# Kernel optimization log

Measured on AMD Instinct MI355X. Metric: run time of the kernel, lower is better.

## Reference

```python
import jax, jax.numpy as jnp
import numpy as np

N, E, IN, H, D = 100000, 1600000, 128, 4, 64
NEG_SLOPE = 0.2
K_APPNP, ALPHA = 5, 0.5
BN_EPS = 1e-5


def setup_inputs() -> dict:
    key = jax.random.key(0)
    ks = jax.random.split(key, 12)
    return {
        'node_feats': jax.random.normal(ks[0], (N, IN), jnp.float32),
        'src': jax.random.randint(ks[1], (E,), 0, N, jnp.int32),
        'dst': jax.random.randint(ks[2], (E,), 0, N, jnp.int32),
        'W_fc': jax.random.normal(ks[3], (IN, H * D), jnp.float32) * (1.0 / np.sqrt(IN)),
        'attn_l': jax.random.normal(ks[4], (H, D), jnp.float32) * 0.1,
        'attn_r': jax.random.normal(ks[5], (H, D), jnp.float32) * 0.1,
        'W_res_gat': jax.random.normal(ks[6], (IN, H * D), jnp.float32) * (1.0 / np.sqrt(IN)),
        'gat_bias': jax.random.normal(ks[7], (H * D,), jnp.float32) * 0.01,
        'conv_w': jax.random.normal(ks[8], (1, H), jnp.float32) * 0.5,
        'conv_b': jax.random.normal(ks[9], (1,), jnp.float32) * 0.01,
        'W_res': jax.random.normal(ks[10], (D, IN), jnp.float32) * (1.0 / np.sqrt(IN)),
        'b_res': jax.random.normal(ks[11], (D,), jnp.float32) * 0.01,
        'gamma': jnp.ones((D,), jnp.float32),
        'beta': jnp.zeros((D,), jnp.float32),
    }


def reference(node_feats, src, dst, W_fc, attn_l, attn_r, W_res_gat, gat_bias,
              conv_w, conv_b, W_res, b_res, gamma, beta):
    # ---- GATConv (4 heads, residual, relu) ----
    feat = (node_feats @ W_fc).reshape(N, H, D)            # (N,H,D)
    el = jnp.einsum('nhd,hd->nh', feat, attn_l)            # (N,H)
    er = jnp.einsum('nhd,hd->nh', feat, attn_r)
    e = jax.nn.leaky_relu(el[src] + er[dst], NEG_SLOPE)    # (E,H)
    # edge softmax over incoming edges of each dst node
    emax = jax.ops.segment_max(e, dst, num_segments=N)     # (N,H)
    emax = jnp.where(jnp.isfinite(emax), emax, 0.0)
    ee = jnp.exp(e - emax[dst])                            # (E,H)
    denom = jax.ops.segment_sum(ee, dst, num_segments=N)   # (N,H)
    a = ee / jnp.maximum(denom[dst], 1e-9)                 # (E,H)
    msg = feat[src] * a[..., None]                         # (E,H,D)
    rst = jax.ops.segment_sum(msg, dst, num_segments=N)    # (N,H,D)
    resval = (node_feats @ W_res_gat).reshape(N, H, D)
    rst = jax.nn.relu(rst + resval + gat_bias.reshape(1, H, D))
    # ---- Conv1d (heads -> 1, kernel_size=1) then flatten ----
    h = jnp.einsum('nhd,oh->nod', rst, conv_w) + conv_b[None, :, None]
    h = h.reshape(N, D)
    # ---- APPNP (k=5, alpha=0.5), symmetric deg^{-1/2} norm (in-degree, clamp 1) ----
    deg = jax.ops.segment_sum(jnp.ones((E,), jnp.float32), dst, num_segments=N)
    norm = jnp.power(jnp.maximum(deg, 1.0), -0.5)[:, None]  # (N,1)
    h0 = h
    for _ in range(K_APPNP):
        h = jax.ops.segment_sum((h * norm)[src], dst, num_segments=N) * norm
        h = (1.0 - ALPHA) * h + ALPHA * h0
    # ---- residual linear + relu ----
    h = h + jax.nn.relu(node_feats @ W_res.T + b_res)
    # ---- BatchNorm1d (batch stats, affine) ----
    mu = h.mean(axis=0)
    var = h.var(axis=0)
    return (h - mu) * jax.lax.rsqrt(var + BN_EPS) * gamma + beta
```

## Files before the change

kernel.cpp:

```cpp
#include <hip/hip_runtime.h>
#include <math.h>

#define NN 100000
#define NE 1600000
#define NEG_SLOPE 0.2f

typedef __attribute__((ext_vector_type(8))) short bf16x8;
typedef __attribute__((ext_vector_type(4))) float f32x4;
typedef __attribute__((ext_vector_type(2))) float f32x2;

__device__ __forceinline__ float b2f(unsigned short u) {
  union { unsigned u; float f; } c; c.u = ((unsigned)u) << 16; return c.f;
}
__device__ __forceinline__ unsigned short f2b(float x) {
  union { float f; unsigned u; } c; c.f = x;
  unsigned r = c.u + 0x7FFFu + ((c.u >> 16) & 1u);
  return (unsigned short)(r >> 16);
}
__device__ __forceinline__ float readlane_f(float v, int l) {
  return __uint_as_float((unsigned)__builtin_amdgcn_readlane((int)__float_as_uint(v), l));
}
__device__ __forceinline__ void fma4(float4& acc, float s, const float4& b) {
  acc.x = fmaf(s, b.x, acc.x);
  acc.y = fmaf(s, b.y, acc.y);
  acc.z = fmaf(s, b.z, acc.z);
  acc.w = fmaf(s, b.w, acc.w);
}
__device__ __forceinline__ float wred(float v) {
#pragma unroll
  for (int off = 32; off > 0; off >>= 1) v += __shfl_xor(v, off, 64);
  return v;
}

__global__ __launch_bounds__(256) void k_zero(int* __restrict__ p, int nwords) {
  int i = blockIdx.x * 256 + threadIdx.x;
  if (i < nwords) p[i] = 0;
}

__global__ void k_zrow(unsigned short* __restrict__ a, unsigned short* __restrict__ b) {
  int i = threadIdx.x;
  a[(size_t)NN * 64 + i] = 0;
  b[(size_t)NN * 64 + i] = 0;
}

__global__ __launch_bounds__(256) void k_cast(const float* __restrict__ A, unsigned short* __restrict__ Ab) {
  int i = blockIdx.x * 256 + threadIdx.x;
  int i4 = i * 4;
  if (i4 < NN * 128) {
    float4 v = *(const float4*)&A[i4];
    ushort4 o; o.x = f2b(v.x); o.y = f2b(v.y); o.z = f2b(v.z); o.w = f2b(v.w);
    *(ushort4*)&Ab[i4] = o;
  }
}

__global__ __launch_bounds__(256) void k_deg(const int* __restrict__ dst, int* __restrict__ deg) {
  int i = blockIdx.x * 256 + threadIdx.x;
  if (i < NE) atomicAdd(&deg[dst[i]], 1);
}

__global__ __launch_bounds__(256) void k_alloc(const int* __restrict__ deg, int* __restrict__ row_start,
                                               int* __restrict__ counter, float* __restrict__ nrm) {
  int i = blockIdx.x * 256 + threadIdx.x;
  if (i < NN) {
    row_start[i] = atomicAdd(counter, deg[i]);
    nrm[i] = rsqrtf(fmaxf((float)deg[i], 1.0f));
  }
}

__global__ __launch_bounds__(256) void k_scatter(const int* __restrict__ src, const int* __restrict__ dst,
                                                 const int* __restrict__ row_start, int* __restrict__ cursor,
                                                 int* __restrict__ csr_src) {
  int i = blockIdx.x * 256 + threadIdx.x;
  if (i < NE) {
    int n = dst[i];
    int p = atomicAdd(&cursor[n], 1);
    csr_src[row_start[n] + p] = src[i];
  }
}

__global__ __launch_bounds__(256) void k_prepw(const float* __restrict__ W_fc, const float* __restrict__ al,
                                               const float* __restrict__ ar, float* __restrict__ w) {
  int o = blockIdx.x * 256 + threadIdx.x;
  if (o >= 1024) return;
  int side = o >> 9;
  int h = (o >> 7) & 3;
  int k = o & 127;
  const float* a = side ? ar : al;
  float s = 0.f;
  for (int d = 0; d < 64; ++d) s += W_fc[k * 256 + h * 64 + d] * a[h * 64 + d];
  w[(side * 4 + h) * 128 + k] = s;
}

__global__ __launch_bounds__(256) void k_elr2(const float* __restrict__ X, const float* __restrict__ w,
                                              float* __restrict__ el, float* __restrict__ er) {
  int n = blockIdx.x * 32 + (threadIdx.x >> 3);
  int p = threadIdx.x & 7;
  if (n >= NN) return;
  const float4* xr = (const float4*)(X + (size_t)n * 128);
  const float4* wr = (const float4*)(w + p * 128);
  float s = 0.f;
#pragma unroll
  for (int i = 0; i < 32; ++i) {
    float4 x = xr[i], ww = wr[i];
    s += x.x * ww.x + x.y * ww.y + x.z * ww.z + x.w * ww.w;
  }
  if (p < 4) el[n * 4 + p] = s;
  else er[n * 4 + (p - 4)] = s;
}

__global__ __launch_bounds__(256) void k_prepB(const float* __restrict__ W_fc, const float* __restrict__ W_rg,
                                               unsigned short* __restrict__ Bp) {
  int y = blockIdx.y;
  const float* Bsrc = (y >> 1) ? W_rg : W_fc;
  int colbase = (y & 1) * 128;
  for (int e = blockIdx.x * 256 + threadIdx.x; e < 16384; e += 2048) {
    int n = e & 127, k = e >> 7;
    int p = colbase + n;
    int d = p >> 2, hh = p & 3;
    float v = Bsrc[k * 256 + hh * 64 + d];
    int nt = n >> 4, nn = n & 15, kt = k >> 5, quad = (k >> 3) & 3, j = k & 7;
    Bp[(size_t)y * 16384 + ((nt * 4 + kt) * 64 + quad * 16 + nn) * 8 + j] = f2b(v);
  }
}

__global__ __launch_bounds__(256) void k_gemm_mfma(const unsigned short* __restrict__ Abf,
                                                   const unsigned short* __restrict__ Bp,
                                                   unsigned* __restrict__ feat8u,
                                                   unsigned short* __restrict__ resval2) {
  __shared__ unsigned short Bl[16384];
  int tid = threadIdx.x;
  int half = blockIdx.y >> 1;
  int colbase = (blockIdx.y & 1) * 128;
  {
    const uint4* src = (const uint4*)(Bp + (size_t)blockIdx.y * 16384);
    uint4* dst4 = (uint4*)Bl;
#pragma unroll
    for (int i = 0; i < 8; ++i) dst4[tid + i * 256] = src[tid + i * 256];
  }
  __syncthreads();
  int w = tid >> 6, lane = tid & 63;
  int quad = lane >> 4;
  int row0 = blockIdx.x * 128;
  int mrow = row0 + (lane & 15);
  f32x4 acc[8][2];
#pragma unroll
  for (int rt = 0; rt < 8; ++rt)
#pragma unroll
    for (int c = 0; c < 2; ++c) acc[rt][c] = (f32x4){0.f, 0.f, 0.f, 0.f};
#pragma unroll
  for (int kt = 0; kt < 4; ++kt) {
    bf16x8 b0 = *(const bf16x8*)&Bl[(((w * 2 + 0) * 4 + kt) * 64 + lane) * 8];
    bf16x8 b1 = *(const bf16x8*)&Bl[(((w * 2 + 1) * 4 + kt) * 64 + lane) * 8];
    int kb = kt * 32 + quad * 8;
#pragma unroll
    for (int rt = 0; rt < 8; ++rt) {
      int rr = mrow + rt * 16; if (rr > NN - 1) rr = NN - 1;
      bf16x8 a = *(const bf16x8*)&Abf[(size_t)rr * 128 + kb];
      acc[rt][0] = __builtin_amdgcn_mfma_f32_16x16x32_bf16(b0, a, acc[rt][0], 0, 0, 0);
      acc[rt][1] = __builtin_amdgcn_mfma_f32_16x16x32_bf16(b1, a, acc[rt][1], 0, 0, 0);
    }
  }
#pragma unroll
  for (int rt = 0; rt < 8; ++rt) {
    int m = row0 + rt * 16 + (lane & 15);
    if (m < NN) {
#pragma unroll
      for (int c = 0; c < 2; ++c) {
        int col = colbase + (w * 2 + c) * 16 + quad * 4;
        if (half == 0) {
          int pk = __builtin_amdgcn_cvt_pk_fp8_f32(acc[rt][c][0], acc[rt][c][1], 0, false);
          pk = __builtin_amdgcn_cvt_pk_fp8_f32(acc[rt][c][2], acc[rt][c][3], pk, true);
          feat8u[(size_t)m * 64 + (col >> 2)] = (unsigned)pk;
        } else {
          ushort4 o;
          o.x = f2b(acc[rt][c][0]); o.y = f2b(acc[rt][c][1]);
          o.z = f2b(acc[rt][c][2]); o.w = f2b(acc[rt][c][3]);
          *(ushort4*)&resval2[(size_t)m * 256 + col] = o;
        }
      }
    }
  }
}

__global__ __launch_bounds__(256) void k_gemm_nt_bias_relu(const float* __restrict__ A, const float* __restrict__ B,
                                                           const float* __restrict__ bias, float* __restrict__ C) {
  __shared__ float Bl[128][68];
  for (int idx = threadIdx.x; idx < 64 * 128; idx += 256) {
    int d = idx >> 7, k = idx & 127;
    Bl[k][d] = B[d * 128 + k];
  }
  __syncthreads();
  int tx = threadIdx.x & 15, ty = threadIdx.x >> 4;
  int row0 = blockIdx.x * 64 + ty * 4;
  const float* ap[4];
#pragma unroll
  for (int r = 0; r < 4; ++r) ap[r] = A + (size_t)min(row0 + r, NN - 1) * 128;
  float4 acc[4];
#pragma unroll
  for (int r = 0; r < 4; ++r) acc[r] = make_float4(0.f, 0.f, 0.f, 0.f);
#pragma unroll 2
  for (int k0 = 0; k0 < 128; k0 += 4) {
    float4 b0 = *(const float4*)&Bl[k0][tx * 4];
    float4 b1 = *(const float4*)&Bl[k0 + 1][tx * 4];
    float4 b2 = *(const float4*)&Bl[k0 + 2][tx * 4];
    float4 b3 = *(const float4*)&Bl[k0 + 3][tx * 4];
#pragma unroll
    for (int r = 0; r < 4; ++r) {
      float4 a = *(const float4*)(ap[r] + k0);
      fma4(acc[r], a.x, b0); fma4(acc[r], a.y, b1);
      fma4(acc[r], a.z, b2); fma4(acc[r], a.w, b3);
    }
  }
  float4 bv = *(const float4*)&bias[tx * 4];
#pragma unroll
  for (int r = 0; r < 4; ++r) {
    int row = row0 + r;
    if (row < NN) {
      float4 v;
      v.x = fmaxf(acc[r].x + bv.x, 0.f);
      v.y = fmaxf(acc[r].y + bv.y, 0.f);
      v.z = fmaxf(acc[r].z + bv.z, 0.f);
      v.w = fmaxf(acc[r].w + bv.w, 0.f);
      *(float4*)&C[(size_t)row * 64 + tx * 4] = v;
    }
  }
}

__global__ __launch_bounds__(256) void k_gat(const int* __restrict__ row_start, const int* __restrict__ deg,
                                             const int* __restrict__ csr_src, const float* __restrict__ el,
                                             const float* __restrict__ er, const unsigned* __restrict__ feat8u,
                                             const unsigned short* __restrict__ resval2,
                                             const float* __restrict__ gat_bias, const float* __restrict__ conv_w,
                                             const float* __restrict__ conv_b, const float* __restrict__ nrm,
                                             float* __restrict__ h0, unsigned short* __restrict__ hsA) {
  int n = blockIdx.x * 4 + (threadIdx.x >> 6);
  int lane = threadIdx.x & 63;
  if (n >= NN) return;
  int s0 = row_start[n], cnt = deg[n];
  float4 er4 = *(const float4*)&er[n * 4];
  f32x2 acc01 = (f32x2){0.f, 0.f}, acc23 = (f32x2){0.f, 0.f};
  float den0 = 0.f, den1 = 0.f, den2 = 0.f, den3 = 0.f;
  for (int base = 0; base < cnt; base += 64) {
    int j = base + lane;
    int s = 0;
    float x0 = 0.f, x1 = 0.f, x2 = 0.f, x3 = 0.f;
    if (j < cnt) {
      s = csr_src[s0 + j];
      float4 el4 = *(const float4*)&el[s * 4];
      float e0 = el4.x + er4.x; e0 = (e0 > 0.f) ? e0 : NEG_SLOPE * e0;
      float e1 = el4.y + er4.y; e1 = (e1 > 0.f) ? e1 : NEG_SLOPE * e1;
      float e2 = el4.z + er4.z; e2 = (e2 > 0.f) ? e2 : NEG_SLOPE * e2;
      float e3 = el4.w + er4.w; e3 = (e3 > 0.f) ? e3 : NEG_SLOPE * e3;
      x0 = __expf(e0); x1 = __expf(e1); x2 = __expf(e2); x3 = __expf(e3);
      den0 += x0; den1 += x1; den2 += x2; den3 += x3;
    }
    int m = cnt - base; if (m > 64) m = 64;
    int mr = (m + 3) & ~3;
    for (int t = 0; t < mr; t += 4) {
      int ss0 = __builtin_amdgcn_readlane(s, t);
      int ss1 = __builtin_amdgcn_readlane(s, t + 1);
      int ss2 = __builtin_amdgcn_readlane(s, t + 2);
      int ss3 = __builtin_amdgcn_readlane(s, t + 3);
      unsigned f0 = feat8u[(size_t)ss0 * 64 + lane];
      unsigned f1 = feat8u[(size_t)ss1 * 64 + lane];
      unsigned f2 = feat8u[(size_t)ss2 * 64 + lane];
      unsigned f3 = feat8u[(size_t)ss3 * 64 + lane];
      {
        f32x2 a01 = (f32x2){readlane_f(x0, t), readlane_f(x1, t)};
        f32x2 a23 = (f32x2){readlane_f(x2, t), readlane_f(x3, t)};
        f32x2 lo = __builtin_amdgcn_cvt_pk_f32_fp8((int)f0, false);
        f32x2 hi = __builtin_amdgcn_cvt_pk_f32_fp8((int)f0, true);
        acc01 += a01 * lo; acc23 += a23 * hi;
      }
      {
        f32x2 a01 = (f32x2){readlane_f(x0, t + 1), readlane_f(x1, t + 1)};
        f32x2 a23 = (f32x2){readlane_f(x2, t + 1), readlane_f(x3, t + 1)};
        f32x2 lo = __builtin_amdgcn_cvt_pk_f32_fp8((int)f1, false);
        f32x2 hi = __builtin_amdgcn_cvt_pk_f32_fp8((int)f1, true);
        acc01 += a01 * lo; acc23 += a23 * hi;
      }
      {
        f32x2 a01 = (f32x2){readlane_f(x0, t + 2), readlane_f(x1, t + 2)};
        f32x2 a23 = (f32x2){readlane_f(x2, t + 2), readlane_f(x3, t + 2)};
        f32x2 lo = __builtin_amdgcn_cvt_pk_f32_fp8((int)f2, false);
        f32x2 hi = __builtin_amdgcn_cvt_pk_f32_fp8((int)f2, true);
        acc01 += a01 * lo; acc23 += a23 * hi;
      }
      {
        f32x2 a01 = (f32x2){readlane_f(x0, t + 3), readlane_f(x1, t + 3)};
        f32x2 a23 = (f32x2){readlane_f(x2, t + 3), readlane_f(x3, t + 3)};
        f32x2 lo = __builtin_amdgcn_cvt_pk_f32_fp8((int)f3, false);
        f32x2 hi = __builtin_amdgcn_cvt_pk_f32_fp8((int)f3, true);
        acc01 += a01 * lo; acc23 += a23 * hi;
      }
    }
  }
  den0 = wred(den0); den1 = wred(den1); den2 = wred(den2); den3 = wred(den3);
  float i0 = 1.f / fmaxf(den0, 1e-9f);
  float i1 = 1.f / fmaxf(den1, 1e-9f);
  float i2 = 1.f / fmaxf(den2, 1e-9f);
  float i3 = 1.f / fmaxf(den3, 1e-9f);
  ushort4 rv = *(const ushort4*)&resval2[(size_t)n * 256 + lane * 4];
  float hmix = conv_b[0];
  float t0;
  t0 = fmaf(acc01.x, i0, b2f(rv.x) + gat_bias[lane]);       t0 = fmaxf(t0, 0.f); hmix = fmaf(conv_w[0], t0, hmix);
  t0 = fmaf(acc01.y, i1, b2f(rv.y) + gat_bias[64 + lane]);  t0 = fmaxf(t0, 0.f); hmix = fmaf(conv_w[1], t0, hmix);
  t0 = fmaf(acc23.x, i2, b2f(rv.z) + gat_bias[128 + lane]); t0 = fmaxf(t0, 0.f); hmix = fmaf(conv_w[2], t0, hmix);
  t0 = fmaf(acc23.y, i3, b2f(rv.w) + gat_bias[192 + lane]); t0 = fmaxf(t0, 0.f); hmix = fmaf(conv_w[3], t0, hmix);
  size_t o = (size_t)n * 64 + lane;
  h0[o] = hmix;
  hsA[o] = f2b(hmix * nrm[n]);
}

__global__ __launch_bounds__(256) void k_gather_mid(const int* __restrict__ row_start, const int* __restrict__ deg,
                                                    const int* __restrict__ csr_src,
                                                    const unsigned short* __restrict__ hs_in,
                                                    const float* __restrict__ nrm, const float* __restrict__ h0,
                                                    unsigned short* __restrict__ hs_out) {
  int n = blockIdx.x * 4 + (threadIdx.x >> 6);
  int lane = threadIdx.x & 63;
  if (n >= NN) return;
  int s0 = row_start[n], cnt = deg[n];
  float acc = 0.f;
  for (int base = 0; base < cnt; base += 64) {
    int j = base + lane;
    int s = (j < cnt) ? csr_src[s0 + j] : NN;
    int m = cnt - base; if (m > 64) m = 64;
    int mr = (m + 7) & ~7;
    for (int t = 0; t < mr; t += 8) {
      int ss0 = __builtin_amdgcn_readlane(s, t);
      int ss1 = __builtin_amdgcn_readlane(s, t + 1);
      int ss2 = __builtin_amdgcn_readlane(s, t + 2);
      int ss3 = __builtin_amdgcn_readlane(s, t + 3);
      int ss4 = __builtin_amdgcn_readlane(s, t + 4);
      int ss5 = __builtin_amdgcn_readlane(s, t + 5);
      int ss6 = __builtin_amdgcn_readlane(s, t + 6);
      int ss7 = __builtin_amdgcn_readlane(s, t + 7);
      float u0 = b2f(hs_in[(size_t)ss0 * 64 + lane]);
      float u1 = b2f(hs_in[(size_t)ss1 * 64 + lane]);
      float u2 = b2f(hs_in[(size_t)ss2 * 64 + lane]);
      float u3 = b2f(hs_in[(size_t)ss3 * 64 + lane]);
      float u4 = b2f(hs_in[(size_t)ss4 * 64 + lane]);
      float u5 = b2f(hs_in[(size_t)ss5 * 64 + lane]);
      float u6 = b2f(hs_in[(size_t)ss6 * 64 + lane]);
      float u7 = b2f(hs_in[(size_t)ss7 * 64 + lane]);
      acc += ((u0 + u1) + (u2 + u3)) + ((u4 + u5) + (u6 + u7));
    }
  }
  size_t o = (size_t)n * 64 + lane;
  float nn_ = nrm[n];
  float v = fmaf(0.5f * nn_, acc, 0.5f * h0[o]);
  hs_out[o] = f2b(v * nn_);
}

__global__ __launch_bounds__(256) void k_gather_last(const int* __restrict__ row_start, const int* __restrict__ deg,
                                                     const int* __restrict__ csr_src,
                                                     const unsigned short* __restrict__ hs_in,
                                                     const float* __restrict__ nrm, const float* __restrict__ h0,
                                                     unsigned short* __restrict__ hout) {
  int n = blockIdx.x * 4 + (threadIdx.x >> 6);
  int lane = threadIdx.x & 63;
  if (n >= NN) return;
  int s0 = row_start[n], cnt = deg[n];
  float acc = 0.f;
  for (int base = 0; base < cnt; base += 64) {
    int j = base + lane;
    int s = (j < cnt) ? csr_src[s0 + j] : NN;
    int m = cnt - base; if (m > 64) m = 64;
    int mr = (m + 7) & ~7;
    for (int t = 0; t < mr; t += 8) {
      int ss0 = __builtin_amdgcn_readlane(s, t);
      int ss1 = __builtin_amdgcn_readlane(s, t + 1);
      int ss2 = __builtin_amdgcn_readlane(s, t + 2);
      int ss3 = __builtin_amdgcn_readlane(s, t + 3);
      int ss4 = __builtin_amdgcn_readlane(s, t + 4);
      int ss5 = __builtin_amdgcn_readlane(s, t + 5);
      int ss6 = __builtin_amdgcn_readlane(s, t + 6);
      int ss7 = __builtin_amdgcn_readlane(s, t + 7);
      float u0 = b2f(hs_in[(size_t)ss0 * 64 + lane]);
      float u1 = b2f(hs_in[(size_t)ss1 * 64 + lane]);
      float u2 = b2f(hs_in[(size_t)ss2 * 64 + lane]);
      float u3 = b2f(hs_in[(size_t)ss3 * 64 + lane]);
      float u4 = b2f(hs_in[(size_t)ss4 * 64 + lane]);
      float u5 = b2f(hs_in[(size_t)ss5 * 64 + lane]);
      float u6 = b2f(hs_in[(size_t)ss6 * 64 + lane]);
      float u7 = b2f(hs_in[(size_t)ss7 * 64 + lane]);
      acc += ((u0 + u1) + (u2 + u3)) + ((u4 + u5) + (u6 + u7));
    }
  }
  size_t o = (size_t)n * 64 + lane;
  float v = fmaf(0.5f * nrm[n], acc, 0.5f * h0[o]);
  hout[o] = f2b(v);
}

__global__ __launch_bounds__(256) void k_finred(const unsigned short* __restrict__ hl,
                                                const float* __restrict__ res2, float* __restrict__ hfin,
                                                float* __restrict__ bn) {
  __shared__ float s1[256], s2[256];
  int d = threadIdx.x & 63;
  int rb = blockIdx.x * 64;
  float sum = 0.f, sq = 0.f;
  for (int r = threadIdx.x >> 6; r < 64; r += 4) {
    int n = rb + r;
    if (n < NN) {
      size_t idx = (size_t)n * 64 + d;
      float v = b2f(hl[idx]) + res2[idx];
      hfin[idx] = v;
      sum += v; sq += v * v;
    }
  }
  s1[threadIdx.x] = sum; s2[threadIdx.x] = sq;
  __syncthreads();
  if (threadIdx.x < 128) { s1[threadIdx.x] += s1[threadIdx.x + 128]; s2[threadIdx.x] += s2[threadIdx.x + 128]; }
  __syncthreads();
  if (threadIdx.x < 64) {
    atomicAdd(&bn[d], s1[threadIdx.x] + s1[threadIdx.x + 64]);
    atomicAdd(&bn[64 + d], s2[threadIdx.x] + s2[threadIdx.x + 64]);
  }
}

__global__ void k_bnstats(const float* __restrict__ bn, const float* __restrict__ gamma,
                          const float* __restrict__ beta, float* __restrict__ bns) {
  int d = threadIdx.x;
  float mu = bn[d] * (1.0f / NN);
  float var = fmaxf(bn[64 + d] * (1.0f / NN) - mu * mu, 0.f);
  float sc = rsqrtf(var + 1e-5f) * gamma[d];
  bns[d] = sc;
  bns[64 + d] = beta[d] - mu * sc;
}

__global__ __launch_bounds__(256) void k_bnapply(const float* __restrict__ h, const float* __restrict__ bns,
                                                 float* __restrict__ out) {
  int i = blockIdx.x * 256 + threadIdx.x;
  if (i < NN * 64) {
    int d = i & 63;
    out[i] = fmaf(h[i], bns[d], bns[64 + d]);
  }
}

extern "C" void kernel_launch(void* const* d_in, const int* in_sizes, int n_in,
                              void* d_out, int out_size, void* d_ws, size_t ws_size,
                              hipStream_t stream) {
  const float* node_feats = (const float*)d_in[0];
  const int* src = (const int*)d_in[1];
  const int* dst = (const int*)d_in[2];
  const float* W_fc = (const float*)d_in[3];
  const float* attn_l = (const float*)d_in[4];
  const float* attn_r = (const float*)d_in[5];
  const float* W_res_gat = (const float*)d_in[6];
  const float* gat_bias = (const float*)d_in[7];
  const float* conv_w = (const float*)d_in[8];
  const float* conv_b = (const float*)d_in[9];
  const float* W_res = (const float*)d_in[10];
  const float* b_res = (const float*)d_in[11];
  const float* gamma = (const float*)d_in[12];
  const float* beta = (const float*)d_in[13];
  float* out = (float*)d_out;

  char* base = (char*)d_ws;
  size_t off = 0;
  auto alloc = [&](size_t bytes) -> char* {
    char* p = base + off;
    off = (off + bytes + 255) & ~(size_t)255;
    return p;
  };
  unsigned* feat8u        = (unsigned*)alloc((size_t)NN * 256);
  unsigned short* resval2 = (unsigned short*)alloc((size_t)NN * 256 * 2);
  float* res2             = (float*)resval2;
  float* el               = (float*)alloc((size_t)NN * 4 * 4);
  float* er               = (float*)alloc((size_t)NN * 4 * 4);
  float* h0               = (float*)alloc((size_t)NN * 64 * 4);
  unsigned short* Abf     = (unsigned short*)h0;
  unsigned short* hsA     = (unsigned short*)alloc((size_t)(NN + 1) * 64 * 2);
  unsigned short* hsB     = (unsigned short*)alloc((size_t)(NN + 1) * 64 * 2);
  unsigned short* hout    = (unsigned short*)alloc((size_t)NN * 64 * 2);
  int* csr_src            = (int*)alloc((size_t)NE * 4);
  float* nrm              = (float*)alloc((size_t)NN * 4);
  int* row_start          = (int*)alloc((size_t)NN * 4);
  unsigned short* Bpacked = (unsigned short*)alloc((size_t)4 * 16384 * 2);
  float* w_elr            = (float*)alloc((size_t)8 * 128 * 4);
  size_t zoff = off;
  int* deg                = (int*)alloc((size_t)NN * 4);
  int* cursor             = (int*)alloc((size_t)NN * 4);
  int* counter            = (int*)alloc(256);
  float* bn               = (float*)alloc(256 * 4);
  float* hfin             = h0;

  int zwords = (int)((off - zoff) / 4);
  int gE = (NE + 255) / 256;
  int gN = (NN + 255) / 256;
  int gW = (NN + 3) / 4;
  int gM = (NN + 63) / 64;
  int gV = (NN * 64 + 255) / 256;

  k_zero<<<(zwords + 255) / 256, 256, 0, stream>>>((int*)(base + zoff), zwords);
  k_zrow<<<1, 64, 0, stream>>>(hsA, hsB);
  k_deg<<<gE, 256, 0, stream>>>(dst, deg);
  k_alloc<<<gN, 256, 0, stream>>>(deg, row_start, counter, nrm);
  k_scatter<<<gE, 256, 0, stream>>>(src, dst, row_start, cursor, csr_src);

  k_cast<<<(NN * 128 / 4 + 255) / 256, 256, 0, stream>>>(node_feats, Abf);
  k_prepB<<<dim3(8, 4), 256, 0, stream>>>(W_fc, W_res_gat, Bpacked);
  k_prepw<<<4, 256, 0, stream>>>(W_fc, attn_l, attn_r, w_elr);
  k_gemm_mfma<<<dim3((NN + 127) / 128, 4), 256, 0, stream>>>(Abf, Bpacked, feat8u, resval2);

  k_elr2<<<(NN + 31) / 32, 256, 0, stream>>>(node_feats, w_elr, el, er);
  k_gat<<<gW, 256, 0, stream>>>(row_start, deg, csr_src, el, er, feat8u, resval2,
                                gat_bias, conv_w, conv_b, nrm, h0, hsA);

  k_gemm_nt_bias_relu<<<gM, 256, 0, stream>>>(node_feats, W_res, b_res, res2);

  k_gather_mid<<<gW, 256, 0, stream>>>(row_start, deg, csr_src, hsA, nrm, h0, hsB);
  k_gather_mid<<<gW, 256, 0, stream>>>(row_start, deg, csr_src, hsB, nrm, h0, hsA);
  k_gather_mid<<<gW, 256, 0, stream>>>(row_start, deg, csr_src, hsA, nrm, h0, hsB);
  k_gather_mid<<<gW, 256, 0, stream>>>(row_start, deg, csr_src, hsB, nrm, h0, hsA);
  k_gather_last<<<gW, 256, 0, stream>>>(row_start, deg, csr_src, hsA, nrm, h0, hout);

  k_finred<<<gM, 256, 0, stream>>>(hout, res2, hfin, bn);
  k_bnstats<<<1, 64, 0, stream>>>(bn, gamma, beta, bn + 128);
  k_bnapply<<<gV, 256, 0, stream>>>(hfin, bn + 128, out);
}
```

Measured before the change: 841.5 us.

## Gather multiple edges per wave with wide loads and fuse residual into last hop

The GAT and APPNP gather kernels now split each wave into sub-groups that each handle a different edge. Lanes load 8-byte chunks of a neighbour row instead of one element per lane, and the per-edge source indices and attention weights are staged through LDS instead of readlane broadcasts. Partial sums are combined with cross-lane shuffles at the end. The final APPNP hop now adds the residual directly and writes fp32 in place into h0, which removes the separate bf16 hout buffer and one read/write pass from the BN reduction kernel. The LDS staging is done without explicit barriers, which relies on wave-synchronous execution within each wave's private slice.

```diff
diff --git a/kernel.cpp b/kernel.cpp
--- a/kernel.cpp
+++ b/kernel.cpp
@@ -16,9 +16,6 @@
   union { float f; unsigned u; } c; c.f = x;
   unsigned r = c.u + 0x7FFFu + ((c.u >> 16) & 1u);
   return (unsigned short)(r >> 16);
-}
-__device__ __forceinline__ float readlane_f(float v, int l) {
-  return __uint_as_float((unsigned)__builtin_amdgcn_readlane((int)__float_as_uint(v), l));
 }
 __device__ __forceinline__ void fma4(float4& acc, float s, const float4& b) {
   acc.x = fmaf(s, b.x, acc.x);
@@ -233,12 +230,17 @@
                                              const float* __restrict__ gat_bias, const float* __restrict__ conv_w,
                                              const float* __restrict__ conv_b, const float* __restrict__ nrm,
                                              float* __restrict__ h0, unsigned short* __restrict__ hsA) {
-  int n = blockIdx.x * 4 + (threadIdx.x >> 6);
-  int lane = threadIdx.x & 63;
+  __shared__ int s_src[4][64];
+  __shared__ float s_x[4][64][4];
+  int wid = threadIdx.x >> 6, lane = threadIdx.x & 63;
+  int n = blockIdx.x * 4 + wid;
   if (n >= NN) return;
   int s0 = row_start[n], cnt = deg[n];
   float4 er4 = *(const float4*)&er[n * 4];
-  f32x2 acc01 = (f32x2){0.f, 0.f}, acc23 = (f32x2){0.f, 0.f};
+  int k = lane & 31, g = lane >> 5;
+  unsigned koff = (unsigned)(k << 3);
+  f32x2 a01_0 = (f32x2){0.f, 0.f}, a23_0 = (f32x2){0.f, 0.f};
+  f32x2 a01_1 = (f32x2){0.f, 0.f}, a23_1 = (f32x2){0.f, 0.f};
   float den0 = 0.f, den1 = 0.f, den2 = 0.f, den3 = 0.f;
   for (int base = 0; base < cnt; base += 64) {
     int j = base + lane;
@@ -254,45 +256,32 @@
       x0 = __expf(e0); x1 = __expf(e1); x2 = __expf(e2); x3 = __expf(e3);
       den0 += x0; den1 += x1; den2 += x2; den3 += x3;
     }
+    s_src[wid][lane] = s;
+    *(float4*)&s_x[wid][lane][0] = make_float4(x0, x1, x2, x3);
     int m = cnt - base; if (m > 64) m = 64;
     int mr = (m + 3) & ~3;
     for (int t = 0; t < mr; t += 4) {
-      int ss0 = __builtin_amdgcn_readlane(s, t);
-      int ss1 = __builtin_amdgcn_readlane(s, t + 1);
-      int ss2 = __builtin_amdgcn_readlane(s, t + 2);
-      int ss3 = __builtin_amdgcn_readlane(s, t + 3);
-      unsigned f0 = feat8u[(size_t)ss0 * 64 + lane];
-      unsigned f1 = feat8u[(size_t)ss1 * 64 + lane];
-      unsigned f2 = feat8u[(size_t)ss2 * 64 + lane];
-      unsigned f3 = feat8u[(size_t)ss3 * 64 + lane];
-      {
-        f32x2 a01 = (f32x2){readlane_f(x0, t), readlane_f(x1, t)};
-        f32x2 a23 = (f32x2){readlane_f(x2, t), readlane_f(x3, t)};
-        f32x2 lo = __builtin_amdgcn_cvt_pk_f32_fp8((int)f0, false);
-        f32x2 hi = __builtin_amdgcn_cvt_pk_f32_fp8((int)f0, true);
-        acc01 += a01 * lo; acc23 += a23 * hi;
-      }
-      {
-        f32x2 a01 = (f32x2){readlane_f(x0, t + 1), readlane_f(x1, t + 1)};
-        f32x2 a23 = (f32x2){readlane_f(x2, t + 1), readlane_f(x3, t + 1)};
-        f32x2 lo = __builtin_amdgcn_cvt_pk_f32_fp8((int)f1, false);
-        f32x2 hi = __builtin_amdgcn_cvt_pk_f32_fp8((int)f1, true);
-        acc01 += a01 * lo; acc23 += a23 * hi;
-      }
-      {
-        f32x2 a01 = (f32x2){readlane_f(x0, t + 2), readlane_f(x1, t + 2)};
-        f32x2 a23 = (f32x2){readlane_f(x2, t + 2), readlane_f(x3, t + 2)};
-        f32x2 lo = __builtin_amdgcn_cvt_pk_f32_fp8((int)f2, false);
-        f32x2 hi = __builtin_amdgcn_cvt_pk_f32_fp8((int)f2, true);
-        acc01 += a01 * lo; acc23 += a23 * hi;
-      }
-      {
-        f32x2 a01 = (f32x2){readlane_f(x0, t + 3), readlane_f(x1, t + 3)};
-        f32x2 a23 = (f32x2){readlane_f(x2, t + 3), readlane_f(x3, t + 3)};
-        f32x2 lo = __builtin_amdgcn_cvt_pk_f32_fp8((int)f3, false);
-        f32x2 hi = __builtin_amdgcn_cvt_pk_f32_fp8((int)f3, true);
-        acc01 += a01 * lo; acc23 += a23 * hi;
-      }
+      int sA = s_src[wid][t + g];
+      int sB = s_src[wid][t + 2 + g];
+      float4 xA = *(const float4*)&s_x[wid][t + g][0];
+      float4 xB = *(const float4*)&s_x[wid][t + 2 + g][0];
+      uint2 fA = *(const uint2*)((const char*)feat8u + (((unsigned)sA << 8) + koff));
+      uint2 fB = *(const uint2*)((const char*)feat8u + (((unsigned)sB << 8) + koff));
+      f32x2 xa01 = (f32x2){xA.x, xA.y}, xa23 = (f32x2){xA.z, xA.w};
+      f32x2 xb01 = (f32x2){xB.x, xB.y}, xb23 = (f32x2){xB.z, xB.w};
+      f32x2 lo, hi;
+      lo = __builtin_amdgcn_cvt_pk_f32_fp8((int)fA.x, false);
+      hi = __builtin_amdgcn_cvt_pk_f32_fp8((int)fA.x, true);
+      a01_0 += xa01 * lo; a23_0 += xa23 * hi;
+      lo = __builtin_amdgcn_cvt_pk_f32_fp8((int)fA.y, false);
+      hi = __builtin_amdgcn_cvt_pk_f32_fp8((int)fA.y, true);
+      a01_1 += xa01 * lo; a23_1 += xa23 * hi;
+      lo = __builtin_amdgcn_cvt_pk_f32_fp8((int)fB.x, false);
+      hi = __builtin_amdgcn_cvt_pk_f32_fp8((int)fB.x, true);
+      a01_0 += xb01 * lo; a23_0 += xb23 * hi;
+      lo = __builtin_amdgcn_cvt_pk_f32_fp8((int)fB.y, false);
+      hi = __builtin_amdgcn_cvt_pk_f32_fp8((int)fB.y, true);
+      a01_1 += xb01 * lo; a23_1 += xb23 * hi;
     }
   }
   den0 = wred(den0); den1 = wred(den1); den2 = wred(den2); den3 = wred(den3);
@@ -300,16 +289,74 @@
   float i1 = 1.f / fmaxf(den1, 1e-9f);
   float i2 = 1.f / fmaxf(den2, 1e-9f);
   float i3 = 1.f / fmaxf(den3, 1e-9f);
-  ushort4 rv = *(const ushort4*)&resval2[(size_t)n * 256 + lane * 4];
-  float hmix = conv_b[0];
-  float t0;
-  t0 = fmaf(acc01.x, i0, b2f(rv.x) + gat_bias[lane]);       t0 = fmaxf(t0, 0.f); hmix = fmaf(conv_w[0], t0, hmix);
-  t0 = fmaf(acc01.y, i1, b2f(rv.y) + gat_bias[64 + lane]);  t0 = fmaxf(t0, 0.f); hmix = fmaf(conv_w[1], t0, hmix);
-  t0 = fmaf(acc23.x, i2, b2f(rv.z) + gat_bias[128 + lane]); t0 = fmaxf(t0, 0.f); hmix = fmaf(conv_w[2], t0, hmix);
-  t0 = fmaf(acc23.y, i3, b2f(rv.w) + gat_bias[192 + lane]); t0 = fmaxf(t0, 0.f); hmix = fmaf(conv_w[3], t0, hmix);
-  size_t o = (size_t)n * 64 + lane;
-  h0[o] = hmix;
-  hsA[o] = f2b(hmix * nrm[n]);
+  a01_0[0] += __shfl_xor(a01_0[0], 32, 64);
+  a01_0[1] += __shfl_xor(a01_0[1], 32, 64);
+  a23_0[0] += __shfl_xor(a23_0[0], 32, 64);
+  a23_0[1] += __shfl_xor(a23_0[1], 32, 64);
+  a01_1[0] += __shfl_xor(a01_1[0], 32, 64);
+  a01_1[1] += __shfl_xor(a01_1[1], 32, 64);
+  a23_1[0] += __shfl_xor(a23_1[0], 32, 64);
+  a23_1[1] += __shfl_xor(a23_1[1], 32, 64);
+  if (lane < 32) {
+    int d0 = k << 1;
+    uint4 rv = *(const uint4*)&resval2[(size_t)n * 256 + ((unsigned)k << 3)];
+    float2 bb0 = *(const float2*)&gat_bias[d0];
+    float2 bb1 = *(const float2*)&gat_bias[64 + d0];
+    float2 bb2 = *(const float2*)&gat_bias[128 + d0];
+    float2 bb3 = *(const float2*)&gat_bias[192 + d0];
+    float cb = conv_b[0];
+    float cw0 = conv_w[0], cw1 = conv_w[1], cw2 = conv_w[2], cw3 = conv_w[3];
+    float t, hm0 = cb, hm1 = cb;
+    t = fmaf(a01_0[0], i0, b2f((unsigned short)(rv.x & 0xffffu)) + bb0.x); t = fmaxf(t, 0.f); hm0 = fmaf(cw0, t, hm0);
+    t = fmaf(a01_0[1], i1, b2f((unsigned short)(rv.x >> 16)) + bb1.x);     t = fmaxf(t, 0.f); hm0 = fmaf(cw1, t, hm0);
+    t = fmaf(a23_0[0], i2, b2f((unsigned short)(rv.y & 0xffffu)) + bb2.x); t = fmaxf(t, 0.f); hm0 = fmaf(cw2, t, hm0);
+    t = fmaf(a23_0[1], i3, b2f((unsigned short)(rv.y >> 16)) + bb3.x);     t = fmaxf(t, 0.f); hm0 = fmaf(cw3, t, hm0);
+    t = fmaf(a01_1[0], i0, b2f((unsigned short)(rv.z & 0xffffu)) + bb0.y); t = fmaxf(t, 0.f); hm1 = fmaf(cw0, t, hm1);
+    t = fmaf(a01_1[1], i1, b2f((unsigned short)(rv.z >> 16)) + bb1.y);     t = fmaxf(t, 0.f); hm1 = fmaf(cw1, t, hm1);
+    t = fmaf(a23_1[0], i2, b2f((unsigned short)(rv.w & 0xffffu)) + bb2.y); t = fmaxf(t, 0.f); hm1 = fmaf(cw2, t, hm1);
+    t = fmaf(a23_1[1], i3, b2f((unsigned short)(rv.w >> 16)) + bb3.y);     t = fmaxf(t, 0.f); hm1 = fmaf(cw3, t, hm1);
+    float nn_ = nrm[n];
+    size_t o = (size_t)n * 64 + d0;
+    *(float2*)&h0[o] = make_float2(hm0, hm1);
+    ushort2 hs; hs.x = f2b(hm0 * nn_); hs.y = f2b(hm1 * nn_);
+    *(ushort2*)&hsA[o] = hs;
+  }
+}
+
+__device__ __forceinline__ void gather_accum(const int* __restrict__ row_start, const int* __restrict__ deg,
+                                             const int* __restrict__ csr_src,
+                                             const unsigned short* __restrict__ hs_in,
+                                             int n, int wid, int lane,
+                                             float& a0, float& a1, float& a2, float& a3) {
+  __shared__ int s_src[4][64];
+  int s0 = row_start[n], cnt = deg[n];
+  int k = lane & 15, g = lane >> 4;
+  unsigned koff = (unsigned)(k << 3);
+  a0 = 0.f; a1 = 0.f; a2 = 0.f; a3 = 0.f;
+  for (int base = 0; base < cnt; base += 64) {
+    int j = base + lane;
+    s_src[wid][lane] = (j < cnt) ? csr_src[s0 + j] : NN;
+    int m = cnt - base; if (m > 64) m = 64;
+    int mr = (m + 7) & ~7;
+    for (int t = 0; t < mr; t += 8) {
+      int sA = s_src[wid][t + g];
+      int sB = s_src[wid][t + 4 + g];
+      uint2 uA = *(const uint2*)((const char*)hs_in + (((unsigned)sA << 7) + koff));
+      uint2 uB = *(const uint2*)((const char*)hs_in + (((unsigned)sB << 7) + koff));
+      a0 += __uint_as_float(uA.x << 16);
+      a1 += __uint_as_float(uA.x & 0xFFFF0000u);
+      a2 += __uint_as_float(uA.y << 16);
+      a3 += __uint_as_float(uA.y & 0xFFFF0000u);
+      a0 += __uint_as_float(uB.x << 16);
+      a1 += __uint_as_float(uB.x & 0xFFFF0000u);
+      a2 += __uint_as_float(uB.y << 16);
+      a3 += __uint_as_float(uB.y & 0xFFFF0000u);
+    }
+  }
+  a0 += __shfl_xor(a0, 16, 64); a1 += __shfl_xor(a1, 16, 64);
+  a2 += __shfl_xor(a2, 16, 64); a3 += __shfl_xor(a3, 16, 64);
+  a0 += __shfl_xor(a0, 32, 64); a1 += __shfl_xor(a1, 32, 64);
+  a2 += __shfl_xor(a2, 32, 64); a3 += __shfl_xor(a3, 32, 64);
 }
 
 __global__ __launch_bounds__(256) void k_gather_mid(const int* __restrict__ row_start, const int* __restrict__ deg,
@@ -317,85 +364,52 @@
                                                     const unsigned short* __restrict__ hs_in,
                                                     const float* __restrict__ nrm, const float* __restrict__ h0,
                                                     unsigned short* __restrict__ hs_out) {
-  int n = blockIdx.x * 4 + (threadIdx.x >> 6);
-  int lane = threadIdx.x & 63;
+  int wid = threadIdx.x >> 6, lane = threadIdx.x & 63;
+  int n = blockIdx.x * 4 + wid;
   if (n >= NN) return;
-  int s0 = row_start[n], cnt = deg[n];
-  float acc = 0.f;
-  for (int base = 0; base < cnt; base += 64) {
-    int j = base + lane;
-    int s = (j < cnt) ? csr_src[s0 + j] : NN;
-    int m = cnt - base; if (m > 64) m = 64;
-    int mr = (m + 7) & ~7;
-    for (int t = 0; t < mr; t += 8) {
-      int ss0 = __builtin_amdgcn_readlane(s, t);
-      int ss1 = __builtin_amdgcn_readlane(s, t + 1);
-      int ss2 = __builtin_amdgcn_readlane(s, t + 2);
-      int ss3 = __builtin_amdgcn_readlane(s, t + 3);
-      int ss4 = __builtin_amdgcn_readlane(s, t + 4);
-      int ss5 = __builtin_amdgcn_readlane(s, t + 5);
-      int ss6 = __builtin_amdgcn_readlane(s, t + 6);
-      int ss7 = __builtin_amdgcn_readlane(s, t + 7);
-      float u0 = b2f(hs_in[(size_t)ss0 * 64 + lane]);
-      float u1 = b2f(hs_in[(size_t)ss1 * 64 + lane]);
-      float u2 = b2f(hs_in[(size_t)ss2 * 64 + lane]);
-      float u3 = b2f(hs_in[(size_t)ss3 * 64 + lane]);
-      float u4 = b2f(hs_in[(size_t)ss4 * 64 + lane]);
-      float u5 = b2f(hs_in[(size_t)ss5 * 64 + lane]);
-      float u6 = b2f(hs_in[(size_t)ss6 * 64 + lane]);
-      float u7 = b2f(hs_in[(size_t)ss7 * 64 + lane]);
-      acc += ((u0 + u1) + (u2 + u3)) + ((u4 + u5) + (u6 + u7));
-    }
-  }
-  size_t o = (size_t)n * 64 + lane;
-  float nn_ = nrm[n];
-  float v = fmaf(0.5f * nn_, acc, 0.5f * h0[o]);
-  hs_out[o] = f2b(v * nn_);
+  float a0, a1, a2, a3;
+  gather_accum(row_start, deg, csr_src, hs_in, n, wid, lane, a0, a1, a2, a3);
+  if (lane < 16) {
+    size_t o = (size_t)n * 64 + (lane << 2);
+    float nn_ = nrm[n];
+    float4 h4 = *(const float4*)&h0[o];
+    float hn = 0.5f * nn_;
+    float v0 = fmaf(hn, a0, 0.5f * h4.x) * nn_;
+    float v1 = fmaf(hn, a1, 0.5f * h4.y) * nn_;
+    float v2 = fmaf(hn, a2, 0.5f * h4.z) * nn_;
+    float v3 = fmaf(hn, a3, 0.5f * h4.w) * nn_;
+    ushort4 ov; ov.x = f2b(v0); ov.y = f2b(v1); ov.z = f2b(v2); ov.w = f2b(v3);
+    *(ushort4*)&hs_out[o] = ov;
+  }
 }
 
 __global__ __launch_bounds__(256) void k_gather_last(const int* __restrict__ row_start, const int* __restrict__ deg,
                                                      const int* __restrict__ csr_src,
                                                      const unsigned short* __restrict__ hs_in,
-                                                     const float* __restrict__ nrm, const float* __restrict__ h0,
-                                                     unsigned short* __restrict__ hout) {
-  int n = blockIdx.x * 4 + (threadIdx.x >> 6);
-  int lane = threadIdx.x & 63;
+                                                     const float* __restrict__ nrm,
+                                                     const float* __restrict__ res2,
+                                                     float* h0io) {
+  int wid = threadIdx.x >> 6, lane = threadIdx.x & 63;
+  int n = blockIdx.x * 4 + wid;
   if (n >= NN) return;
-  int s0 = row_start[n], cnt = deg[n];
-  float acc = 0.f;
-  for (int base = 0; base < cnt; base += 64) {
-    int j = base + lane;
-    int s = (j < cnt) ? csr_src[s0 + j] : NN;
-    int m = cnt - base; if (m > 64) m = 64;
-    int mr = (m + 7) & ~7;
-    for (int t = 0; t < mr; t += 8) {
-      int ss0 = __builtin_amdgcn_readlane(s, t);
-      int ss1 = __builtin_amdgcn_readlane(s, t + 1);
-      int ss2 = __builtin_amdgcn_readlane(s, t + 2);
-      int ss3 = __builtin_amdgcn_readlane(s, t + 3);
-      int ss4 = __builtin_amdgcn_readlane(s, t + 4);
-      int ss5 = __builtin_amdgcn_readlane(s, t + 5);
-      int ss6 = __builtin_amdgcn_readlane(s, t + 6);
-      int ss7 = __builtin_amdgcn_readlane(s, t + 7);
-      float u0 = b2f(hs_in[(size_t)ss0 * 64 + lane]);
-      float u1 = b2f(hs_in[(size_t)ss1 * 64 + lane]);
-      float u2 = b2f(hs_in[(size_t)ss2 * 64 + lane]);
-      float u3 = b2f(hs_in[(size_t)ss3 * 64 + lane]);
-      float u4 = b2f(hs_in[(size_t)ss4 * 64 + lane]);
-      float u5 = b2f(hs_in[(size_t)ss5 * 64 + lane]);
-      float u6 = b2f(hs_in[(size_t)ss6 * 64 + lane]);
-      float u7 = b2f(hs_in[(size_t)ss7 * 64 + lane]);
-      acc += ((u0 + u1) + (u2 + u3)) + ((u4 + u5) + (u6 + u7));
-    }
-  }
-  size_t o = (size_t)n * 64 + lane;
-  float v = fmaf(0.5f * nrm[n], acc, 0.5f * h0[o]);
-  hout[o] = f2b(v);
-}
-
-__global__ __launch_bounds__(256) void k_finred(const unsigned short* __restrict__ hl,
-                                                const float* __restrict__ res2, float* __restrict__ hfin,
-                                                float* __restrict__ bn) {
+  float a0, a1, a2, a3;
+  gather_accum(row_start, deg, csr_src, hs_in, n, wid, lane, a0, a1, a2, a3);
+  if (lane < 16) {
+    size_t o = (size_t)n * 64 + (lane << 2);
+    float nn_ = nrm[n];
+    float4 h4 = *(const float4*)&h0io[o];
+    float4 r4 = *(const float4*)&res2[o];
+    float hn = 0.5f * nn_;
+    float4 v;
+    v.x = fmaf(hn, a0, 0.5f * h4.x) + r4.x;
+    v.y = fmaf(hn, a1, 0.5f * h4.y) + r4.y;
+    v.z = fmaf(hn, a2, 0.5f * h4.z) + r4.z;
+    v.w = fmaf(hn, a3, 0.5f * h4.w) + r4.w;
+    *(float4*)&h0io[o] = v;
+  }
+}
+
+__global__ __launch_bounds__(256) void k_finred(const float* __restrict__ hfin, float* __restrict__ bn) {
   __shared__ float s1[256], s2[256];
   int d = threadIdx.x & 63;
   int rb = blockIdx.x * 64;
@@ -403,9 +417,7 @@
   for (int r = threadIdx.x >> 6; r < 64; r += 4) {
     int n = rb + r;
     if (n < NN) {
-      size_t idx = (size_t)n * 64 + d;
-      float v = b2f(hl[idx]) + res2[idx];
-      hfin[idx] = v;
+      float v = hfin[(size_t)n * 64 + d];
       sum += v; sq += v * v;
     }
   }
@@ -473,7 +485,6 @@
   unsigned short* Abf     = (unsigned short*)h0;
   unsigned short* hsA     = (unsigned short*)alloc((size_t)(NN + 1) * 64 * 2);
   unsigned short* hsB     = (unsigned short*)alloc((size_t)(NN + 1) * 64 * 2);
-  unsigned short* hout    = (unsigned short*)alloc((size_t)NN * 64 * 2);
   int* csr_src            = (int*)alloc((size_t)NE * 4);
   float* nrm              = (float*)alloc((size_t)NN * 4);
   int* row_start          = (int*)alloc((size_t)NN * 4);
@@ -514,9 +525,9 @@
   k_gather_mid<<<gW, 256, 0, stream>>>(row_start, deg, csr_src, hsB, nrm, h0, hsA);
   k_gather_mid<<<gW, 256, 0, stream>>>(row_start, deg, csr_src, hsA, nrm, h0, hsB);
   k_gather_mid<<<gW, 256, 0, stream>>>(row_start, deg, csr_src, hsB, nrm, h0, hsA);
-  k_gather_last<<<gW, 256, 0, stream>>>(row_start, deg, csr_src, hsA, nrm, h0, hout);
-
-  k_finred<<<gM, 256, 0, stream>>>(hout, res2, hfin, bn);
+  k_gather_last<<<gW, 256, 0, stream>>>(row_start, deg, csr_src, hsA, nrm, res2, hfin);
+
+  k_finred<<<gM, 256, 0, stream>>>(hfin, bn);
   k_bnstats<<<1, 64, 0, stream>>>(bn, gamma, beta, bn + 128);
   k_bnapply<<<gV, 256, 0, stream>>>(hfin, bn + 128, out);
 }
```

Measured after the change: 834.9 us. About the same (-0.8%).
